# Kernel tuning notes

Measured on AMD Instinct MI355X. Metric: run time of the kernel, lower is better.

The kernel has to match this reference:

```python
import jax, jax.numpy as jnp
import numpy as np

# dimensions
N = 50000    # nodes
E = 600000   # edges
NS = 64      # scalar (0e) channels of node features
NV = 32      # vector (1o) channels of node features
A = 16       # node attr channels (16x0e)
R = 8        # edge embedding dim (radial basis, 8x0e)
H = 8        # fc_hidden_size
AVG_NB = 12.0  # avg_num_neighbors
# gate layout: NS scalars (silu) + NV gate scalars (sigmoid) gating NV vectors
GS = NS + NV  # 96 scalar channels before gate
NW = NS + NS + NV + NV  # 192 per-edge TP weights (paths: s*Y0->0e, s*Y1->1o, v*Y0->1o, v.Y1->0e)


def setup_inputs() -> dict:
    key = jax.random.key(0)
    ks = jax.random.split(key, 20)
    d = {
        'node_s': jax.random.normal(ks[0], (N, NS), jnp.float32),
        'node_v': jax.random.normal(ks[1], (N, NV, 3), jnp.float32),
        'node_attrs': jax.random.normal(ks[2], (N, A), jnp.float32),
        'edge_emb': jax.random.uniform(ks[3], (E, R), jnp.float32),
        'edge_sh0': jnp.ones((E, 1), jnp.float32),
        'edge_sh1': jax.random.normal(ks[4], (E, 3), jnp.float32),
        'edge_index': jax.random.randint(ks[5], (2, E), 0, N),
        # linear_1 on node feats (per-irrep channel mixing)
        'W1s': jax.random.normal(ks[6], (NS, NS), jnp.float32),
        'W1v': jax.random.normal(ks[7], (NV, NV), jnp.float32),
        # radial MLP producing per-edge TP weights
        'Wm1': jax.random.normal(ks[8], (R, H), jnp.float32),
        'Wm2': jax.random.normal(ks[9], (H, NW), jnp.float32),
        # linear_2: TP out (96x0e+96x1o) -> pre-gate (96x0e+32x1o)
        'W2s': jax.random.normal(ks[10], (GS, GS), jnp.float32),
        'W2v': jax.random.normal(ks[11], (NS + NV, NV), jnp.float32),
        # update UVU TP internal weights (msg x attrs)
        'Wt0': jax.random.normal(ks[12], (NS, A), jnp.float32),
        'Wt1': jax.random.normal(ks[13], (NV, A), jnp.float32),
        # linear_3
        'W3s': jax.random.normal(ks[14], (NS, GS), jnp.float32),
        'W3v': jax.random.normal(ks[15], (NV, NV), jnp.float32),
        # self connection: FullyConnectedTensorProduct(node_feats, attrs -> pre-gate)
        'Wsc0': jax.random.normal(ks[16], (NS, A, GS), jnp.float32),
        'Wsc1': jax.random.normal(ks[17], (NV, A, NV), jnp.float32),
    }
    return d


def _gate(s_all, v):
    # s_all: [.., GS]; first NS scalars -> silu, last NV -> sigmoid gates for vectors
    scal = jax.nn.silu(s_all[..., :NS])
    gates = jax.nn.sigmoid(s_all[..., NS:])
    return scal, v * gates[..., None]


def reference(node_s, node_v, node_attrs, edge_emb, edge_sh0, edge_sh1, edge_index,
              W1s, W1v, Wm1, Wm2, W2s, W2v, Wt0, Wt1, W3s, W3v, Wsc0, Wsc1):
    src, dst = edge_index[0], edge_index[1]

    # ---- message ----
    s1 = (node_s @ W1s) / jnp.sqrt(jnp.float32(NS))                       # [N,NS]
    v1 = jnp.einsum('nuc,uv->nvc', node_v, W1v) / jnp.sqrt(jnp.float32(NV))
    ss = s1[src]   # [E,NS]
    vv = v1[src]   # [E,NV,3]

    # per-edge TP weights from radial MLP
    w = jax.nn.silu(edge_emb @ Wm1) @ Wm2                                 # [E,NW]
    w0a, w1a, w1b, w0b = jnp.split(w, [NS, 2 * NS, 2 * NS + NV], axis=1)

    # UVU tensor product with SH edge attrs (lmax=1)
    t0a = w0a * ss * edge_sh0                                             # [E,NS] 0e
    t0b = w0b * jnp.einsum('euc,ec->eu', vv, edge_sh1)                    # [E,NV] 0e
    t1a = w1a[:, :, None] * ss[:, :, None] * edge_sh1[:, None, :]         # [E,NS,3] 1o
    t1b = w1b[:, :, None] * vv * edge_sh0[:, :, None]                     # [E,NV,3] 1o
    tp_s = jnp.concatenate([t0a, t0b], axis=1)                            # [E,96]
    tp_v = jnp.concatenate([t1a, t1b], axis=1)                            # [E,96,3]

    m_s = (tp_s @ W2s) / jnp.sqrt(jnp.float32(GS))                        # [E,GS]
    m_v = jnp.einsum('euc,uv->evc', tp_v, W2v) / jnp.sqrt(jnp.float32(NS + NV))  # [E,NV,3]
    msg_s, msg_v = _gate(m_s, m_v)                                        # [E,NS], [E,NV,3]

    # ---- update ----
    agg_s = jax.ops.segment_sum(msg_s, dst, num_segments=N) / jnp.sqrt(jnp.float32(AVG_NB))
    agg_v = jax.ops.segment_sum(msg_v, dst, num_segments=N) / jnp.sqrt(jnp.float32(AVG_NB))

    u0 = jnp.einsum('nu,na,ua->nu', agg_s, node_attrs, Wt0) / jnp.sqrt(jnp.float32(A))
    u1 = jnp.einsum('nuc,na,ua->nuc', agg_v, node_attrs, Wt1) / jnp.sqrt(jnp.float32(A))

    f_s = (u0 @ W3s) / jnp.sqrt(jnp.float32(NS))                          # [N,GS]
    f_v = jnp.einsum('nuc,uv->nvc', u1, W3v) / jnp.sqrt(jnp.float32(NV))  # [N,NV,3]

    # self connection (fully connected TP with scalar attrs)
    sc_s = jnp.einsum('nu,na,uav->nv', node_s, node_attrs, Wsc0) / jnp.sqrt(jnp.float32(NS * A))
    sc_v = jnp.einsum('nuc,na,uaw->nwc', node_v, node_attrs, Wsc1) / jnp.sqrt(jnp.float32(NV * A))
    f_s = f_s + sc_s
    f_v = f_v + sc_v

    out_s, out_v = _gate(f_s, f_v)                                        # [N,NS], [N,NV,3]
    return jnp.concatenate([out_s, out_v.reshape(N, NV * 3)], axis=1)     # [N,160]
```

## Files before the change

### kernel.cpp

```cpp
#include <hip/hip_runtime.h>
#include <math.h>

#define N 50000
#define E 600000
#define EPB 16
#define LDK 104

typedef __attribute__((ext_vector_type(8))) short short8;
typedef __attribute__((ext_vector_type(4))) float float4v;

__device__ __forceinline__ float silu_f(float x) { return x / (1.f + __expf(-x)); }
__device__ __forceinline__ float sigm_f(float x) { return 1.f / (1.f + __expf(-x)); }
__device__ __forceinline__ unsigned short f2bf(float f) {
  unsigned u = __float_as_uint(f);
  u += 0x7fff + ((u >> 16) & 1);
  return (unsigned short)(u >> 16);
}
__device__ __forceinline__ float bf2f(unsigned short u) {
  return __uint_as_float(((unsigned)u) << 16);
}

__global__ void k_hist(const int* __restrict__ eidx, int* __restrict__ counts) {
  int e = blockIdx.x * 256 + threadIdx.x;
  if (e < E) atomicAdd(&counts[eidx[E + e]], 1);
}

__global__ __launch_bounds__(1024)
void k_scan(const int* __restrict__ counts, int* __restrict__ row_ptr) {
  __shared__ int ssum[1024];
  const int t = threadIdx.x;
  const int CH = 49;
  int lo = t * CH, hi = min(lo + CH, N);
  int s = 0;
  for (int i = lo; i < hi; i++) s += counts[i];
  ssum[t] = s;
  __syncthreads();
  for (int off = 1; off < 1024; off <<= 1) {
    int v = (t >= off) ? ssum[t - off] : 0;
    __syncthreads();
    ssum[t] += v;
    __syncthreads();
  }
  int run = (t == 0) ? 0 : ssum[t - 1];
  for (int i = lo; i < hi; i++) { row_ptr[i] = run; run += counts[i]; }
  if (t == 1023) row_ptr[N] = ssum[1023];
}

__global__ void k_scatter(const int* __restrict__ eidx, const int* __restrict__ row_ptr,
                          int* __restrict__ woff, int* __restrict__ perm) {
  int e = blockIdx.x * 256 + threadIdx.x;
  if (e < E) {
    int d = eidx[E + e];
    int p = atomicAdd(&woff[d], 1);
    perm[row_ptr[d] + p] = e;
  }
}

__global__ void k_prep(const float* __restrict__ Wsc0, const float* __restrict__ W3s,
                       const float* __restrict__ Wsc1, const float* __restrict__ W3v,
                       const float* __restrict__ W2s, const float* __restrict__ W2v,
                       unsigned short* __restrict__ BT, unsigned short* __restrict__ B2T,
                       unsigned short* __restrict__ w2sTg, unsigned short* __restrict__ w2vTg) {
  const float isq96 = 0.10206207261596575f;
  int i = blockIdx.x * 256 + threadIdx.x;
  if (i < 96 * 1088) {
    int j = i / 1088, k = i % 1088;
    float v;
    if (k < 1024) v = Wsc0[(size_t)k * 96 + j] * 0.03125f;
    else          v = W3s[(size_t)(k - 1024) * 96 + j] * 0.125f;
    BT[i] = f2bf(v);
  } else if (i < 96 * 1088 + 32 * 576) {
    int i2 = i - 96 * 1088;
    int w = i2 / 576, k = i2 % 576;
    float v = 0.f;
    if (k < 512)      v = Wsc1[(size_t)k * 32 + w] * 0.04419417382415922f;
    else if (k < 544) v = W3v[(size_t)(k - 512) * 32 + w] * 0.17677669529663689f;
    B2T[i2] = f2bf(v);
  } else if (i < 96 * 1088 + 32 * 576 + 96 * 96) {
    int i3 = i - (96 * 1088 + 32 * 576);
    int j = i3 / 96, k = i3 % 96;
    w2sTg[i3] = f2bf(W2s[(size_t)k * 96 + j] * isq96);
  } else {
    int i4 = i - (96 * 1088 + 32 * 576 + 96 * 96);
    if (i4 < 32 * 96) {
      int v = i4 / 96, u = i4 % 96;
      w2vTg[i4] = f2bf(W2v[(size_t)u * 32 + v] * isq96);
    }
  }
}

__global__ __launch_bounds__(256, 4)
void k_lin1(const float* __restrict__ node_s, const float* __restrict__ node_v,
            const float* __restrict__ W1s, const float* __restrict__ W1v,
            float* __restrict__ s1, float* __restrict__ v1) {
  __shared__ float w1s[64 * 64];
  __shared__ float w1v[32 * 32];
  for (int i = threadIdx.x; i < 64 * 64; i += 256) w1s[i] = W1s[i];
  for (int i = threadIdx.x; i < 32 * 32; i += 256) w1v[i] = W1v[i];
  __syncthreads();
  const float is_ns = 0.125f;
  const float is_nv = 0.17677669529663689f;
  int gtid = blockIdx.x * 256 + threadIdx.x;
  int stride = gridDim.x * 256;
  for (int i = gtid; i < N * 160; i += stride) {
    int n = i / 160, ch = i % 160;
    if (ch < 64) {
      const float* row = node_s + n * 64;
      float acc = 0.f;
#pragma unroll
      for (int u = 0; u < 64; u++) acc += row[u] * w1s[u * 64 + ch];
      s1[n * 64 + ch] = acc * is_ns;
    } else {
      int p = ch - 64, v = p / 3, c = p % 3;
      const float* row = node_v + n * 96;
      float acc = 0.f;
#pragma unroll
      for (int u = 0; u < 32; u++) acc += row[u * 3 + c] * w1v[u * 32 + v];
      v1[n * 96 + p] = acc * is_nv;
    }
  }
}

template<int STORE>
__global__ __launch_bounds__(256, 4)
void k_msg(const float* __restrict__ s1, const float* __restrict__ v1,
           const float* __restrict__ emb, const float* __restrict__ sh0g,
           const float* __restrict__ sh1g, const int* __restrict__ eidx,
           const float* __restrict__ Wm1, const float* __restrict__ Wm2,
           const unsigned short* __restrict__ w2sTg, const unsigned short* __restrict__ w2vTg,
           float* __restrict__ aggs, float* __restrict__ aggv,
           unsigned short* __restrict__ msgS, unsigned short* __restrict__ msgV) {
  __shared__ float wm2s[192 * 9];
  __shared__ float wm1s[64];
  __shared__ unsigned short tps[EPB * LDK];
  __shared__ unsigned short tpv[EPB * 3 * LDK];
  __shared__ float gat[EPB][33];
  __shared__ float hb[EPB][8];
  __shared__ float sh1b[EPB][4];
  __shared__ float sh0b[EPB];
  __shared__ int ssrc[EPB];
  __shared__ int sdst[EPB];

  const int t = threadIdx.x;
  const int wave = t >> 6, lane = t & 63;
  const int lm = lane & 15, quad = lane >> 4;
  const int subc = t & 15;

  for (int i = t; i < 192 * 8; i += 256) {
    int h = i / 192, c = i % 192;
    wm2s[c * 9 + h] = Wm2[i];
  }
  if (t < 64) wm1s[t] = Wm1[t];

  short8 b1fr[2][3], b2fr[3];
  {
    const int nt0 = wave;
    const int nt1 = (wave + 4 < 6) ? wave + 4 : wave;
    const int nv2 = wave & 1;
#pragma unroll
    for (int kk = 0; kk < 3; kk++) {
      b1fr[0][kk] = *(const short8*)&w2sTg[(nt0 * 16 + lm) * 96 + kk * 32 + quad * 8];
      b1fr[1][kk] = *(const short8*)&w2sTg[(nt1 * 16 + lm) * 96 + kk * 32 + quad * 8];
      b2fr[kk]    = *(const short8*)&w2vTg[(nv2 * 16 + lm) * 96 + kk * 32 + quad * 8];
    }
  }
  __syncthreads();

  for (int pass = blockIdx.x; pass < E / EPB; pass += gridDim.x) {
    const int ebase = pass * EPB;
    __syncthreads();
    if (t < EPB) {
      ssrc[t] = eidx[ebase + t];
      if (!STORE) sdst[t] = eidx[E + ebase + t];
      sh0b[t] = sh0g[ebase + t];
    } else if (t >= 64 && t < 64 + EPB * 3) {
      int i = t - 64;
      sh1b[i / 3][i % 3] = sh1g[ebase * 3 + i];
    } else if (t >= 128) {
      int i = t - 128, el = i >> 3, sub = i & 7;
      float acc = 0.f;
#pragma unroll
      for (int r = 0; r < 8; r++) acc += emb[(ebase + el) * 8 + r] * wm1s[r * 8 + sub];
      hb[el][sub] = silu_f(acc);
    }
    __syncthreads();
    {
      const int el = t >> 4, sub = subc;
      const int src = ssrc[el];
      const float s0v = sh0b[el];
      const float x0 = sh1b[el][0], x1 = sh1b[el][1], x2 = sh1b[el][2];
      float hr[8];
#pragma unroll
      for (int h = 0; h < 8; h++) hr[h] = hb[el][h];
      const float4v ss = *(const float4v*)&s1[(size_t)src * 64 + sub * 4];
      unsigned short tsv[4], tvv[3][4];
#pragma unroll
      for (int i = 0; i < 4; i++) {
        float w0a = 0.f, w1a = 0.f;
#pragma unroll
        for (int h = 0; h < 8; h++) {
          w0a += hr[h] * wm2s[(sub * 4 + i) * 9 + h];
          w1a += hr[h] * wm2s[(64 + sub * 4 + i) * 9 + h];
        }
        const float ssu = ss[i];
        tsv[i] = f2bf(w0a * ssu * s0v);
        const float base = w1a * ssu;
        tvv[0][i] = f2bf(base * x0);
        tvv[1][i] = f2bf(base * x1);
        tvv[2][i] = f2bf(base * x2);
      }
      *(uint2*)&tps[el * LDK + sub * 4] = *(uint2*)tsv;
#pragma unroll
      for (int c = 0; c < 3; c++)
        *(uint2*)&tpv[(el * 3 + c) * LDK + sub * 4] = *(uint2*)tvv[c];
      const float2* vp = (const float2*)&v1[(size_t)src * 96 + sub * 6];
      const float2 va = vp[0], vb = vp[1], vc = vp[2];
      const float v6[6] = {va.x, va.y, vb.x, vb.y, vc.x, vc.y};
      unsigned short ts2[2], tv2[3][2];
#pragma unroll
      for (int i2 = 0; i2 < 2; i2++) {
        float w1b = 0.f, w0b = 0.f;
#pragma unroll
        for (int h = 0; h < 8; h++) {
          w1b += hr[h] * wm2s[(128 + sub * 2 + i2) * 9 + h];
          w0b += hr[h] * wm2s[(160 + sub * 2 + i2) * 9 + h];
        }
        const float vx = v6[i2 * 3 + 0], vy = v6[i2 * 3 + 1], vz = v6[i2 * 3 + 2];
        ts2[i2] = f2bf(w0b * (vx * x0 + vy * x1 + vz * x2));
        tv2[0][i2] = f2bf(w1b * vx * s0v);
        tv2[1][i2] = f2bf(w1b * vy * s0v);
        tv2[2][i2] = f2bf(w1b * vz * s0v);
      }
      *(unsigned*)&tps[el * LDK + 64 + sub * 2] = *(unsigned*)ts2;
#pragma unroll
      for (int c = 0; c < 3; c++)
        *(unsigned*)&tpv[(el * 3 + c) * LDK + 64 + sub * 2] = *(unsigned*)tv2[c];
    }
    __syncthreads();
    {
      short8 afr[3];
#pragma unroll
      for (int kk = 0; kk < 3; kk++)
        afr[kk] = *(const short8*)&tps[lm * LDK + kk * 32 + quad * 8];
#pragma unroll
      for (int t2 = 0; t2 < 2; t2++) {
        const int nt = wave + t2 * 4;
        if (nt < 6) {
          float4v acc = {0.f, 0.f, 0.f, 0.f};
#pragma unroll
          for (int kk = 0; kk < 3; kk++)
            acc = __builtin_amdgcn_mfma_f32_16x16x32_bf16(afr[kk], b1fr[t2][kk], acc, 0, 0, 0);
          const int j = nt * 16 + lm;
#pragma unroll
          for (int reg = 0; reg < 4; reg++) {
            const int e = quad * 4 + reg;
            const float val = acc[reg];
            if (j < 64) {
              if (STORE) msgS[(size_t)(ebase + e) * 64 + j] = f2bf(silu_f(val));
              else atomicAdd(&aggs[(size_t)sdst[e] * 64 + j], silu_f(val));
            } else {
              gat[e][j - 64] = sigm_f(val);
            }
          }
        }
      }
    }
    __syncthreads();
#pragma unroll
    for (int t2 = 0; t2 < 2; t2++) {
      const int tile = wave + t2 * 4;
      if (tile < 6) {
        const int mt = tile >> 1, nt2 = tile & 1;
        float4v acc = {0.f, 0.f, 0.f, 0.f};
#pragma unroll
        for (int kk = 0; kk < 3; kk++) {
          short8 a = *(const short8*)&tpv[(mt * 16 + lm) * LDK + kk * 32 + quad * 8];
          acc = __builtin_amdgcn_mfma_f32_16x16x32_bf16(a, b2fr[kk], acc, 0, 0, 0);
        }
        const int v = nt2 * 16 + lm;
#pragma unroll
        for (int reg = 0; reg < 4; reg++) {
          const int r = mt * 16 + quad * 4 + reg;
          const int e = (r * 171) >> 9, c = r - 3 * e;
          const float val = acc[reg] * gat[e][v];
          if (STORE) msgV[(size_t)(ebase + e) * 96 + v * 3 + c] = f2bf(val);
          else atomicAdd(&aggv[(size_t)sdst[e] * 96 + v * 3 + c], val);
        }
      }
    }
  }
}

__global__ __launch_bounds__(256, 8)
void k_agg(const unsigned short* __restrict__ msgS, const unsigned short* __restrict__ msgV,
           const int* __restrict__ rowp, const int* __restrict__ perm,
           float* __restrict__ aggs, float* __restrict__ aggv) {
  const int wv = threadIdx.x >> 6, lane = threadIdx.x & 63;
  const int n = blockIdx.x * 4 + wv;
  const int lo = rowp[n], hi = rowp[n + 1];
  float sS = 0.f, v0 = 0.f, v1a = 0.f;
  int r = lo;
  for (; r + 2 <= hi; r += 2) {
    const int e0 = perm[r], e1 = perm[r + 1];
    const unsigned short a0 = msgS[(size_t)e0 * 64 + lane];
    const unsigned short a1 = msgS[(size_t)e1 * 64 + lane];
    const unsigned short b0 = msgV[(size_t)e0 * 96 + lane];
    const unsigned short b1 = msgV[(size_t)e1 * 96 + lane];
    unsigned short c0 = 0, c1 = 0;
    if (lane < 32) {
      c0 = msgV[(size_t)e0 * 96 + 64 + lane];
      c1 = msgV[(size_t)e1 * 96 + 64 + lane];
    }
    sS += bf2f(a0) + bf2f(a1);
    v0 += bf2f(b0) + bf2f(b1);
    v1a += bf2f(c0) + bf2f(c1);
  }
  for (; r < hi; r++) {
    const int e0 = perm[r];
    sS += bf2f(msgS[(size_t)e0 * 64 + lane]);
    v0 += bf2f(msgV[(size_t)e0 * 96 + lane]);
    if (lane < 32) v1a += bf2f(msgV[(size_t)e0 * 96 + 64 + lane]);
  }
  aggs[(size_t)n * 64 + lane] = sS;
  aggv[(size_t)n * 96 + lane] = v0;
  if (lane < 32) aggv[(size_t)n * 96 + 64 + lane] = v1a;
}

__global__ __launch_bounds__(256, 4)
void k_c1(const float* __restrict__ node_s, const float* __restrict__ attrs,
          const float* __restrict__ aggs, const float* __restrict__ Wt0,
          const unsigned short* __restrict__ BT,
          float* __restrict__ out, float* __restrict__ gates) {
  __shared__ float s_row[32][64];
  __shared__ float attr[32][16];
  __shared__ float t0[32][64];
  __shared__ float wt0[1024];
  __shared__ unsigned short As[32 * 72];
  const int t = threadIdx.x;
  const int wave = t >> 6, lane = t & 63, lm = lane & 15, quad = lane >> 4;
  const int nbase = blockIdx.x * 32;

  for (int i = t; i < 1024; i += 256) wt0[i] = Wt0[i];
  for (int i = t; i < 2048; i += 256) {
    int nl = i >> 6, u = i & 63, n = nbase + nl;
    s_row[nl][u] = (n < N) ? node_s[(size_t)n * 64 + u] : 0.f;
    t0[nl][u]    = (n < N) ? aggs[(size_t)n * 64 + u] : 0.f;
  }
  for (int i = t; i < 512; i += 256) {
    int nl = i >> 4, a = i & 15, n = nbase + nl;
    attr[nl][a] = (n < N) ? attrs[(size_t)n * 16 + a] : 0.f;
  }
  __syncthreads();
  for (int i = t; i < 2048; i += 256) {
    int nl = i >> 6, u = i & 63;
    float d0 = 0.f;
#pragma unroll
    for (int a = 0; a < 16; a++) d0 += attr[nl][a] * wt0[u * 16 + a];
    t0[nl][u] *= d0 * 0.07216878364870322f;
  }

  float4v acc[3] = {{0,0,0,0},{0,0,0,0},{0,0,0,0}};
  int mts[3], nts[3];
#pragma unroll
  for (int tt = 0; tt < 3; tt++) {
    const int tile = wave + tt * 4;
    mts[tt] = tile / 6;
    nts[tt] = tile % 6;
  }

  for (int kc = 0; kc < 17; kc++) {
    __syncthreads();
    {
      const int row = t >> 3, c0 = (t & 7) * 8;
      unsigned short tmp[8];
      if (kc < 16) {
        const int u = kc * 4 + (c0 >> 4);
        const float sval = s_row[row][u];
        const int ab = c0 & 8;
#pragma unroll
        for (int i = 0; i < 8; i++) tmp[i] = f2bf(sval * attr[row][ab + i]);
      } else {
#pragma unroll
        for (int i = 0; i < 8; i++) tmp[i] = f2bf(t0[row][c0 + i]);
      }
      *(uint4*)&As[row * 72 + c0] = *(uint4*)tmp;
    }
    __syncthreads();
#pragma unroll
    for (int ks = 0; ks < 2; ks++) {
      short8 am0 = *(const short8*)&As[(lm) * 72 + ks * 32 + quad * 8];
      short8 am1 = *(const short8*)&As[(16 + lm) * 72 + ks * 32 + quad * 8];
#pragma unroll
      for (int tt = 0; tt < 3; tt++) {
        short8 b = *(const short8*)&BT[(size_t)(nts[tt] * 16 + lm) * 1088 + kc * 64 + ks * 32 + quad * 8];
        acc[tt] = __builtin_amdgcn_mfma_f32_16x16x32_bf16(mts[tt] ? am1 : am0, b, acc[tt], 0, 0, 0);
      }
    }
  }
#pragma unroll
  for (int tt = 0; tt < 3; tt++) {
    const int j = nts[tt] * 16 + lm;
#pragma unroll
    for (int reg = 0; reg < 4; reg++) {
      const int m = mts[tt] * 16 + quad * 4 + reg;
      const int n = nbase + m;
      if (n < N) {
        const float val = acc[tt][reg];
        if (j < 64) out[(size_t)n * 160 + j] = silu_f(val);
        else        gates[(size_t)n * 32 + (j - 64)] = sigm_f(val);
      }
    }
  }
}

__global__ __launch_bounds__(256, 3)
void k_c2(const float* __restrict__ node_v, const float* __restrict__ attrs,
          const float* __restrict__ aggv, const float* __restrict__ Wt1,
          const unsigned short* __restrict__ B2T, const float* __restrict__ gts,
          float* __restrict__ out) {
  __shared__ float nvs[32][96];
  __shared__ float t1s[32][96];
  __shared__ float attr[32][16];
  __shared__ float wt1[512];
  __shared__ unsigned short As2[96 * 72];
  const int t = threadIdx.x;
  const int wave = t >> 6, lane = t & 63, lm = lane & 15, quad = lane >> 4;
  const int nbase = blockIdx.x * 32;

  for (int i = t; i < 512; i += 256) wt1[i] = Wt1[i];
  for (int i = t; i < 32 * 96; i += 256) {
    int nl = i / 96, rr = i % 96, n = nbase + nl;
    nvs[nl][rr] = (n < N) ? node_v[(size_t)n * 96 + rr] : 0.f;
    t1s[nl][rr] = (n < N) ? aggv[(size_t)n * 96 + rr] : 0.f;
  }
  for (int i = t; i < 512; i += 256) {
    int nl = i >> 4, a = i & 15, n = nbase + nl;
    attr[nl][a] = (n < N) ? attrs[(size_t)n * 16 + a] : 0.f;
  }
  __syncthreads();
  for (int i = t; i < 1024; i += 256) {
    int nl = i >> 5, u = i & 31;
    float d1 = 0.f;
#pragma unroll
    for (int a = 0; a < 16; a++) d1 += attr[nl][a] * wt1[u * 16 + a];
    d1 *= 0.07216878364870322f;
    t1s[nl][u * 3 + 0] *= d1; t1s[nl][u * 3 + 1] *= d1; t1s[nl][u * 3 + 2] *= d1;
  }

  float4v acc[3] = {{0,0,0,0},{0,0,0,0},{0,0,0,0}};
  int mts[3], nts[3];
#pragma unroll
  for (int tt = 0; tt < 3; tt++) {
    const int tile = wave + tt * 4;
    mts[tt] = tile >> 1;
    nts[tt] = tile & 1;
  }

  for (int kc = 0; kc < 9; kc++) {
    __syncthreads();
#pragma unroll
    for (int jj = 0; jj < 3; jj++) {
      const int job = t + jj * 256;
      const int row = job >> 3, c0 = (job & 7) * 8;
      const int nl = (row * 171) >> 9, c = row - 3 * nl;
      const int kbase = kc * 64 + c0;
      unsigned short tmp[8];
      if (kbase < 512) {
        const int u = kbase >> 4;
        const float vval = nvs[nl][u * 3 + c];
        const int ab = c0 & 8;
#pragma unroll
        for (int i = 0; i < 8; i++) tmp[i] = f2bf(vval * attr[nl][ab + i]);
      } else if (kbase < 544) {
        const int u2 = kbase - 512;
#pragma unroll
        for (int i = 0; i < 8; i++) tmp[i] = f2bf(t1s[nl][(u2 + i) * 3 + c]);
      } else {
#pragma unroll
        for (int i = 0; i < 8; i++) tmp[i] = 0;
      }
      *(uint4*)&As2[row * 72 + c0] = *(uint4*)tmp;
    }
    __syncthreads();
#pragma unroll
    for (int ks = 0; ks < 2; ks++) {
#pragma unroll
      for (int tt = 0; tt < 3; tt++) {
        short8 a = *(const short8*)&As2[(mts[tt] * 16 + lm) * 72 + ks * 32 + quad * 8];
        short8 b = *(const short8*)&B2T[(size_t)(nts[tt] * 16 + lm) * 576 + kc * 64 + ks * 32 + quad * 8];
        acc[tt] = __builtin_amdgcn_mfma_f32_16x16x32_bf16(a, b, acc[tt], 0, 0, 0);
      }
    }
  }
#pragma unroll
  for (int tt = 0; tt < 3; tt++) {
    const int w = nts[tt] * 16 + lm;
#pragma unroll
    for (int reg = 0; reg < 4; reg++) {
      const int row = mts[tt] * 16 + quad * 4 + reg;
      const int nl = (row * 171) >> 9, c = row - 3 * nl;
      const int n = nbase + nl;
      if (n < N)
        out[(size_t)n * 160 + 64 + w * 3 + c] = acc[tt][reg] * gts[(size_t)n * 32 + w];
    }
  }
}

extern "C" void kernel_launch(void* const* d_in, const int* in_sizes, int n_in,
                              void* d_out, int out_size, void* d_ws, size_t ws_size,
                              hipStream_t stream) {
  const float* node_s = (const float*)d_in[0];
  const float* node_v = (const float*)d_in[1];
  const float* attrs  = (const float*)d_in[2];
  const float* emb    = (const float*)d_in[3];
  const float* sh0    = (const float*)d_in[4];
  const float* sh1    = (const float*)d_in[5];
  const int*   eidx   = (const int*)d_in[6];
  const float* W1s    = (const float*)d_in[7];
  const float* W1v    = (const float*)d_in[8];
  const float* Wm1    = (const float*)d_in[9];
  const float* Wm2    = (const float*)d_in[10];
  const float* W2s    = (const float*)d_in[11];
  const float* W2v    = (const float*)d_in[12];
  const float* Wt0    = (const float*)d_in[13];
  const float* Wt1    = (const float*)d_in[14];
  const float* W3s    = (const float*)d_in[15];
  const float* W3v    = (const float*)d_in[16];
  const float* Wsc0   = (const float*)d_in[17];
  const float* Wsc1   = (const float*)d_in[18];

  char* p = (char*)d_ws;
  float* s1  = (float*)p;  p += (size_t)N * 64 * 4;
  float* v1f = (float*)p;  p += (size_t)N * 96 * 4;
  float* gts = (float*)p;  p += (size_t)N * 32 * 4;
  unsigned short* BT    = (unsigned short*)p;  p += (size_t)96 * 1088 * 2;
  unsigned short* B2T   = (unsigned short*)p;  p += (size_t)32 * 576 * 2;
  unsigned short* w2sTg = (unsigned short*)p;  p += (size_t)96 * 96 * 2;
  unsigned short* w2vTg = (unsigned short*)p;  p += (size_t)32 * 96 * 2;
  char* pmode = p;
  size_t base = (size_t)(pmode - (char*)d_ws);
  size_t need_store = base + ((size_t)N + 1) * 4 + (size_t)N * 4 + (size_t)E * 4
                    + (size_t)E * 64 * 2 + (size_t)E * 96 * 2;
  const bool store = (ws_size >= need_store);

  k_prep<<<528, 256, 0, stream>>>(Wsc0, W3s, Wsc1, W3v, W2s, W2v, BT, B2T, w2sTg, w2vTg);
  k_lin1<<<1024, 256, 0, stream>>>(node_s, node_v, W1s, W1v, s1, v1f);

  if (store) {
    int* rowp = (int*)pmode;
    int* cnt  = rowp + (N + 1);
    int* perm = cnt + N;
    unsigned short* msgS = (unsigned short*)(perm + E);
    unsigned short* msgV = msgS + (size_t)E * 64;
    hipMemsetAsync(cnt, 0, (size_t)N * 4, stream);
    k_hist<<<(E + 255) / 256, 256, 0, stream>>>(eidx, cnt);
    k_scan<<<1, 1024, 0, stream>>>(cnt, rowp);
    hipMemsetAsync(cnt, 0, (size_t)N * 4, stream);
    k_scatter<<<(E + 255) / 256, 256, 0, stream>>>(eidx, rowp, cnt, perm);
    k_msg<1><<<1024, 256, 0, stream>>>(s1, v1f, emb, sh0, sh1, eidx, Wm1, Wm2,
                                       w2sTg, w2vTg, nullptr, nullptr, msgS, msgV);
    float* aggs = s1;
    float* aggv = v1f;
    k_agg<<<N / 4, 256, 0, stream>>>(msgS, msgV, rowp, perm, aggs, aggv);
    k_c1<<<1563, 256, 0, stream>>>(node_s, attrs, aggs, Wt0, BT, (float*)d_out, gts);
    k_c2<<<1563, 256, 0, stream>>>(node_v, attrs, aggv, Wt1, B2T, gts, (float*)d_out);
  } else {
    float* aggs = (float*)pmode;
    float* aggv = aggs + (size_t)N * 64;
    hipMemsetAsync(aggs, 0, (size_t)N * 160 * 4, stream);
    k_msg<0><<<1024, 256, 0, stream>>>(s1, v1f, emb, sh0, sh1, eidx, Wm1, Wm2,
                                       w2sTg, w2vTg, aggs, aggv, nullptr, nullptr);
    k_c1<<<1563, 256, 0, stream>>>(node_s, attrs, aggs, Wt0, BT, (float*)d_out, gts);
    k_c2<<<1563, 256, 0, stream>>>(node_v, attrs, aggv, Wt1, B2T, gts, (float*)d_out);
  }
}
```

Before: 753.9 us.

## Fuse CSR aggregation with update and self-connection GEMMs into one kernel

Replaces the separate k_agg, k_c1 and k_c2 launches with a single k_upd kernel. Each block gathers the incoming bf16 messages for its 32 nodes, keeps the aggregates and the gate values in shared memory, and runs both scalar and vector MFMA GEMMs before writing the output. This removes the fp32 agg and gate round trips through global memory and two kernel launches. In exchange the block uses much more shared memory (launch bounds drop to 2), which lowers occupancy for the latency-bound gather phase.

```diff
diff --git a/kernel.cpp b/kernel.cpp
--- a/kernel.cpp
+++ b/kernel.cpp
@@ -291,39 +291,202 @@
   }
 }
 
-__global__ __launch_bounds__(256, 8)
-void k_agg(const unsigned short* __restrict__ msgS, const unsigned short* __restrict__ msgV,
+__global__ __launch_bounds__(256, 2)
+void k_upd(const float* __restrict__ node_s, const float* __restrict__ node_v,
+           const float* __restrict__ attrs,
+           const unsigned short* __restrict__ msgS, const unsigned short* __restrict__ msgV,
            const int* __restrict__ rowp, const int* __restrict__ perm,
-           float* __restrict__ aggs, float* __restrict__ aggv) {
-  const int wv = threadIdx.x >> 6, lane = threadIdx.x & 63;
-  const int n = blockIdx.x * 4 + wv;
-  const int lo = rowp[n], hi = rowp[n + 1];
-  float sS = 0.f, v0 = 0.f, v1a = 0.f;
-  int r = lo;
-  for (; r + 2 <= hi; r += 2) {
-    const int e0 = perm[r], e1 = perm[r + 1];
-    const unsigned short a0 = msgS[(size_t)e0 * 64 + lane];
-    const unsigned short a1 = msgS[(size_t)e1 * 64 + lane];
-    const unsigned short b0 = msgV[(size_t)e0 * 96 + lane];
-    const unsigned short b1 = msgV[(size_t)e1 * 96 + lane];
-    unsigned short c0 = 0, c1 = 0;
-    if (lane < 32) {
-      c0 = msgV[(size_t)e0 * 96 + 64 + lane];
-      c1 = msgV[(size_t)e1 * 96 + 64 + lane];
-    }
-    sS += bf2f(a0) + bf2f(a1);
-    v0 += bf2f(b0) + bf2f(b1);
-    v1a += bf2f(c0) + bf2f(c1);
-  }
-  for (; r < hi; r++) {
-    const int e0 = perm[r];
-    sS += bf2f(msgS[(size_t)e0 * 64 + lane]);
-    v0 += bf2f(msgV[(size_t)e0 * 96 + lane]);
-    if (lane < 32) v1a += bf2f(msgV[(size_t)e0 * 96 + 64 + lane]);
-  }
-  aggs[(size_t)n * 64 + lane] = sS;
-  aggv[(size_t)n * 96 + lane] = v0;
-  if (lane < 32) aggv[(size_t)n * 96 + 64 + lane] = v1a;
+           const float* __restrict__ Wt0, const float* __restrict__ Wt1,
+           const unsigned short* __restrict__ BT, const unsigned short* __restrict__ B2T,
+           float* __restrict__ out) {
+  __shared__ float s_row[32][64];
+  __shared__ float nvs[32][96];
+  __shared__ float attr[32][16];
+  __shared__ float t0[32][64];
+  __shared__ float t1s[32][96];
+  __shared__ float gatesL[32][33];
+  __shared__ unsigned short As2[96 * 72];
+  const int t = threadIdx.x;
+  const int wave = t >> 6, lane = t & 63, lm = lane & 15, quad = lane >> 4;
+  const int nbase = blockIdx.x * 32;
+
+  for (int i = t; i < 2048; i += 256) {
+    int nl = i >> 6, u = i & 63, n = nbase + nl;
+    s_row[nl][u] = (n < N) ? node_s[(size_t)n * 64 + u] : 0.f;
+  }
+  for (int i = t; i < 32 * 96; i += 256) {
+    int nl = i / 96, rr = i % 96, n = nbase + nl;
+    nvs[nl][rr] = (n < N) ? node_v[(size_t)n * 96 + rr] : 0.f;
+  }
+  for (int i = t; i < 512; i += 256) {
+    int nl = i >> 4, a = i & 15, n = nbase + nl;
+    attr[nl][a] = (n < N) ? attrs[(size_t)n * 16 + a] : 0.f;
+  }
+
+  for (int k = 0; k < 8; k++) {
+    const int nl = wave * 8 + k;
+    const int n = nbase + nl;
+    float sS = 0.f, v0 = 0.f, v1a = 0.f;
+    if (n < N) {
+      const int lo = rowp[n], hi = rowp[n + 1];
+      int r = lo;
+      for (; r + 2 <= hi; r += 2) {
+        const int e0 = perm[r], e1 = perm[r + 1];
+        const unsigned short a0 = msgS[(size_t)e0 * 64 + lane];
+        const unsigned short a1 = msgS[(size_t)e1 * 64 + lane];
+        const unsigned short b0 = msgV[(size_t)e0 * 96 + lane];
+        const unsigned short b1 = msgV[(size_t)e1 * 96 + lane];
+        unsigned short c0 = 0, c1 = 0;
+        if (lane < 32) {
+          c0 = msgV[(size_t)e0 * 96 + 64 + lane];
+          c1 = msgV[(size_t)e1 * 96 + 64 + lane];
+        }
+        sS += bf2f(a0) + bf2f(a1);
+        v0 += bf2f(b0) + bf2f(b1);
+        v1a += bf2f(c0) + bf2f(c1);
+      }
+      for (; r < hi; r++) {
+        const int e0 = perm[r];
+        sS += bf2f(msgS[(size_t)e0 * 64 + lane]);
+        v0 += bf2f(msgV[(size_t)e0 * 96 + lane]);
+        if (lane < 32) v1a += bf2f(msgV[(size_t)e0 * 96 + 64 + lane]);
+      }
+    }
+    t0[nl][lane] = sS;
+    t1s[nl][lane] = v0;
+    if (lane < 32) t1s[nl][64 + lane] = v1a;
+  }
+  __syncthreads();
+
+  for (int i = t; i < 2048; i += 256) {
+    int nl = i >> 6, u = i & 63;
+    float d0 = 0.f;
+#pragma unroll
+    for (int a = 0; a < 16; a++) d0 += attr[nl][a] * Wt0[u * 16 + a];
+    t0[nl][u] *= d0 * 0.07216878364870322f;
+  }
+  for (int i = t; i < 1024; i += 256) {
+    int nl = i >> 5, u = i & 31;
+    float d1 = 0.f;
+#pragma unroll
+    for (int a = 0; a < 16; a++) d1 += attr[nl][a] * Wt1[u * 16 + a];
+    d1 *= 0.07216878364870322f;
+    t1s[nl][u * 3 + 0] *= d1; t1s[nl][u * 3 + 1] *= d1; t1s[nl][u * 3 + 2] *= d1;
+  }
+
+  {
+    float4v acc[3] = {{0,0,0,0},{0,0,0,0},{0,0,0,0}};
+    int mts[3], nts[3];
+#pragma unroll
+    for (int tt = 0; tt < 3; tt++) {
+      const int tile = wave + tt * 4;
+      mts[tt] = tile / 6;
+      nts[tt] = tile % 6;
+    }
+    for (int kc = 0; kc < 17; kc++) {
+      __syncthreads();
+      {
+        const int row = t >> 3, c0 = (t & 7) * 8;
+        unsigned short tmp[8];
+        if (kc < 16) {
+          const int u = kc * 4 + (c0 >> 4);
+          const float sval = s_row[row][u];
+          const int ab = c0 & 8;
+#pragma unroll
+          for (int i = 0; i < 8; i++) tmp[i] = f2bf(sval * attr[row][ab + i]);
+        } else {
+#pragma unroll
+          for (int i = 0; i < 8; i++) tmp[i] = f2bf(t0[row][c0 + i]);
+        }
+        *(uint4*)&As2[row * 72 + c0] = *(uint4*)tmp;
+      }
+      __syncthreads();
+#pragma unroll
+      for (int ks = 0; ks < 2; ks++) {
+        short8 am0 = *(const short8*)&As2[(lm) * 72 + ks * 32 + quad * 8];
+        short8 am1 = *(const short8*)&As2[(16 + lm) * 72 + ks * 32 + quad * 8];
+#pragma unroll
+        for (int tt = 0; tt < 3; tt++) {
+          short8 b = *(const short8*)&BT[(size_t)(nts[tt] * 16 + lm) * 1088 + kc * 64 + ks * 32 + quad * 8];
+          acc[tt] = __builtin_amdgcn_mfma_f32_16x16x32_bf16(mts[tt] ? am1 : am0, b, acc[tt], 0, 0, 0);
+        }
+      }
+    }
+#pragma unroll
+    for (int tt = 0; tt < 3; tt++) {
+      const int j = nts[tt] * 16 + lm;
+#pragma unroll
+      for (int reg = 0; reg < 4; reg++) {
+        const int m = mts[tt] * 16 + quad * 4 + reg;
+        const int n = nbase + m;
+        const float val = acc[tt][reg];
+        if (j < 64) {
+          if (n < N) out[(size_t)n * 160 + j] = silu_f(val);
+        } else {
+          gatesL[m][j - 64] = sigm_f(val);
+        }
+      }
+    }
+  }
+
+  {
+    float4v acc[3] = {{0,0,0,0},{0,0,0,0},{0,0,0,0}};
+    int mts[3], nts[3];
+#pragma unroll
+    for (int tt = 0; tt < 3; tt++) {
+      const int tile = wave + tt * 4;
+      mts[tt] = tile >> 1;
+      nts[tt] = tile & 1;
+    }
+    for (int kc = 0; kc < 9; kc++) {
+      __syncthreads();
+#pragma unroll
+      for (int jj = 0; jj < 3; jj++) {
+        const int job = t + jj * 256;
+        const int row = job >> 3, c0 = (job & 7) * 8;
+        const int nl = (row * 171) >> 9, c = row - 3 * nl;
+        const int kbase = kc * 64 + c0;
+        unsigned short tmp[8];
+        if (kbase < 512) {
+          const int u = kbase >> 4;
+          const float vval = nvs[nl][u * 3 + c];
+          const int ab = c0 & 8;
+#pragma unroll
+          for (int i = 0; i < 8; i++) tmp[i] = f2bf(vval * attr[nl][ab + i]);
+        } else if (kbase < 544) {
+          const int u2 = kbase - 512;
+#pragma unroll
+          for (int i = 0; i < 8; i++) tmp[i] = f2bf(t1s[nl][(u2 + i) * 3 + c]);
+        } else {
+#pragma unroll
+          for (int i = 0; i < 8; i++) tmp[i] = 0;
+        }
+        *(uint4*)&As2[row * 72 + c0] = *(uint4*)tmp;
+      }
+      __syncthreads();
+#pragma unroll
+      for (int ks = 0; ks < 2; ks++) {
+#pragma unroll
+        for (int tt = 0; tt < 3; tt++) {
+          short8 a = *(const short8*)&As2[(mts[tt] * 16 + lm) * 72 + ks * 32 + quad * 8];
+          short8 b = *(const short8*)&B2T[(size_t)(nts[tt] * 16 + lm) * 576 + kc * 64 + ks * 32 + quad * 8];
+          acc[tt] = __builtin_amdgcn_mfma_f32_16x16x32_bf16(a, b, acc[tt], 0, 0, 0);
+        }
+      }
+    }
+#pragma unroll
+    for (int tt = 0; tt < 3; tt++) {
+      const int w = nts[tt] * 16 + lm;
+#pragma unroll
+      for (int reg = 0; reg < 4; reg++) {
+        const int row = mts[tt] * 16 + quad * 4 + reg;
+        const int nl = (row * 171) >> 9, c = row - 3 * nl;
+        const int n = nbase + nl;
+        if (n < N)
+          out[(size_t)n * 160 + 64 + w * 3 + c] = acc[tt][reg] * gatesL[nl][w];
+      }
+    }
+  }
 }
 
 __global__ __launch_bounds__(256, 4)
@@ -559,11 +722,8 @@
     k_scatter<<<(E + 255) / 256, 256, 0, stream>>>(eidx, rowp, cnt, perm);
     k_msg<1><<<1024, 256, 0, stream>>>(s1, v1f, emb, sh0, sh1, eidx, Wm1, Wm2,
                                        w2sTg, w2vTg, nullptr, nullptr, msgS, msgV);
-    float* aggs = s1;
-    float* aggv = v1f;
-    k_agg<<<N / 4, 256, 0, stream>>>(msgS, msgV, rowp, perm, aggs, aggv);
-    k_c1<<<1563, 256, 0, stream>>>(node_s, attrs, aggs, Wt0, BT, (float*)d_out, gts);
-    k_c2<<<1563, 256, 0, stream>>>(node_v, attrs, aggv, Wt1, B2T, gts, (float*)d_out);
+    k_upd<<<1563, 256, 0, stream>>>(node_s, node_v, attrs, msgS, msgV, rowp, perm,
+                                    Wt0, Wt1, BT, B2T, (float*)d_out);
   } else {
     float* aggs = (float*)pmode;
     float* aggv = aggs + (size_t)N * 64;
```

Result: slower. 898.7 us (+19.2%).
